# Kernel tuning notes

Measured on AMD Instinct MI355X. Metric: run time of the kernel, lower is better.

Reference implementation:

```python
import jax, jax.numpy as jnp
import numpy as np

B, T, IN, OUT, H, N, M = 16, 1024, 64, 64, 512, 128, 40
EPS = 1e-8


def setup_inputs() -> dict:
    key = jax.random.key(0)
    ks = jax.random.split(key, 16)
    s = 0.02  # xavier-ish init scale for weights
    inp = {
        "x": jax.random.normal(ks[0], (B, T, IN), jnp.float32),
        "h0": jnp.zeros((B, H), jnp.float32),
        "c0": jnp.zeros((B, H), jnp.float32),
        "memory0": jax.random.normal(ks[1], (B, N, M), jnp.float32) * 0.01,
        "read0": jnp.zeros((B, M), jnp.float32),
        # LSTMCell params (torch gate order: i, f, g, o)
        "W_ih": jax.random.normal(ks[2], (4 * H, IN + M), jnp.float32) * s,
        "b_ih": jnp.zeros((4 * H,), jnp.float32),
        "W_hh": jax.random.normal(ks[3], (4 * H, H), jnp.float32) * s,
        "b_hh": jnp.zeros((4 * H,), jnp.float32),
        "W_fc": jax.random.normal(ks[4], (OUT, H), jnp.float32) * s,
        "b_fc": jnp.zeros((OUT,), jnp.float32),
        "W_e": jax.random.normal(ks[5], (M, H), jnp.float32) * s,
        "b_e": jnp.zeros((M,), jnp.float32),
        "W_a": jax.random.normal(ks[6], (M, H), jnp.float32) * s,
        "b_a": jnp.zeros((M,), jnp.float32),
        "W_k": jax.random.normal(ks[7], (M, H), jnp.float32) * s,
        "b_k": jnp.zeros((M,), jnp.float32),
        "W_b": jax.random.normal(ks[8], (1, H), jnp.float32) * s,
        "b_b": jnp.zeros((1,), jnp.float32),
    }
    return inp


def _ntm_scan(x, h0, c0, memory0, read0, W_ih, b_ih, W_hh, b_hh,
              W_fc, b_fc, W_e, b_e, W_a, b_a, W_k, b_k, W_b, b_b):
    def step(carry, x_t):
        h, c, mem, r = carry
        # controller LSTM cell on [x_t, read_vector]
        inp = jnp.concatenate([x_t, r], axis=-1)            # [B, IN+M]
        gates = inp @ W_ih.T + b_ih + h @ W_hh.T + b_hh      # [B, 4H]
        i, f, g, o = jnp.split(gates, 4, axis=-1)
        i = jax.nn.sigmoid(i); f = jax.nn.sigmoid(f)
        g = jnp.tanh(g);       o = jax.nn.sigmoid(o)
        c = f * c + i * g
        h = o * jnp.tanh(c)
        out = jnp.tanh(h @ W_fc.T + b_fc)                    # [B, OUT]
        # content addressing
        key = jnp.tanh(h @ W_k.T + b_k)                      # [B, M]
        beta = jax.nn.softplus(h @ W_b.T + b_b) + EPS        # [B, 1]
        kn = key / (jnp.linalg.norm(key, axis=-1, keepdims=True) + EPS)
        mn = mem / (jnp.linalg.norm(mem, axis=-1, keepdims=True) + EPS)
        sim = jnp.einsum('bnm,bm->bn', mn, kn)               # [B, N]
        w = jax.nn.softmax(beta * sim, axis=-1)              # [B, N]
        # erase/add write, then read from updated memory
        e = jax.nn.sigmoid(h @ W_e.T + b_e)                  # [B, M]
        a = jnp.tanh(h @ W_a.T + b_a)                        # [B, M]
        mem = mem * (1.0 - w[:, :, None] * e[:, None, :]) + w[:, :, None] * a[:, None, :]
        r = jnp.einsum('bn,bnm->bm', w, mem)                 # [B, M]
        return (h, c, mem, r), out

    xs = jnp.swapaxes(x, 0, 1)                               # [T, B, IN]
    (h, c, mem, r), outs = jax.lax.scan(step, (h0, c0, memory0, read0), xs)
    return jnp.swapaxes(outs, 0, 1), h, c                    # [B, T, OUT]


def reference(x, h0, c0, memory0, read0, W_ih, b_ih, W_hh, b_hh,
              W_fc, b_fc, W_e, b_e, W_a, b_a, W_k, b_k, W_b, b_b):
    return _ntm_scan(x, h0, c0, memory0, read0, W_ih, b_ih, W_hh, b_hh,
                     W_fc, b_fc, W_e, b_e, W_a, b_a, W_k, b_k, W_b, b_b)
```

## Files before the change

kernel.cpp:

```cpp
#include <hip/hip_runtime.h>
#include <math.h>

#define Bq   16
#define Tq   1024
#define OUTq 64
#define Hq   512
#define Nq   128
#define Mq   40
#define NT   512
#define NISL 16
#define GWG  13
#define IWG  14
#define NWG  224
#define EPSq 1e-8f
#define MAGIC 0x00C0FFEEu

typedef unsigned long long ull;

__device__ __forceinline__ float sigmf(float x){ return 1.f/(1.f + expf(-x)); }
__device__ __forceinline__ float softplusf(float x){ return (x > 20.f) ? x : log1pf(expf(x)); }

__device__ __forceinline__ ull icld64(const ull* p){
  return __hip_atomic_load(p, __ATOMIC_RELAXED, __HIP_MEMORY_SCOPE_AGENT);
}
__device__ __forceinline__ void icst64(ull* p, ull v){
  __hip_atomic_store(p, v, __ATOMIC_RELAXED, __HIP_MEMORY_SCOPE_AGENT);
}
__device__ __forceinline__ ull icpoll64(const ull* p){
  ull v;
  asm volatile("global_load_dwordx2 %0, %1, off sc0 sc1\n\ts_waitcnt vmcnt(0)"
               : "=v"(v) : "v"(p) : "memory");
  return v;
}
__device__ __forceinline__ ull packtv(unsigned tag, float v){
  return ((ull)tag << 32) | (ull)__float_as_uint(v);
}
__device__ __forceinline__ float lowf(ull v){ return __uint_as_float((unsigned)v); }

__device__ __forceinline__ float waitword(const ull* sh, unsigned want, bool fast){
  if (fast){
    #pragma unroll 1
    for (int i = 0; i < 4096; ++i){
      const ull v = icpoll64(sh);
      if ((unsigned)(v >> 32) == want) return lowf(v);
      __builtin_amdgcn_s_sleep(1);
    }
  }
  #pragma unroll 1
  for (;;){
    const ull v = icld64(sh);
    if ((unsigned)(v >> 32) == want) return lowf(v);
    __builtin_amdgcn_s_sleep(1);
  }
}

__device__ __forceinline__ int ready_and_handshake(ull* rdy, ull* magic, int blk){
  __hip_atomic_fetch_add(rdy, 1ull, __ATOMIC_RELAXED, __HIP_MEMORY_SCOPE_AGENT);
  while (icld64(rdy) < (ull)NWG) __builtin_amdgcn_s_sleep(8);
  if (blk == 0) icst64(magic, ((ull)MAGIC << 32) | 1ull);
  #pragma unroll 1
  for (int i = 0; i < 4000; ++i){
    if ((unsigned)(icpoll64(magic) >> 32) == MAGIC) return 1;
    __builtin_amdgcn_s_sleep(2);
  }
  return 0;
}

extern "C" __global__ void __launch_bounds__(NT, 1)
ntm_kernel(const float* __restrict__ xg,  const float* __restrict__ h0g,
           const float* __restrict__ c0g, const float* __restrict__ mem0g,
           const float* __restrict__ read0g,
           const float* __restrict__ Wih, const float* __restrict__ bih,
           const float* __restrict__ Whh, const float* __restrict__ bhh,
           const float* __restrict__ Wfc, const float* __restrict__ bfc,
           const float* __restrict__ We,  const float* __restrict__ be,
           const float* __restrict__ Wa,  const float* __restrict__ ba,
           const float* __restrict__ Wk,  const float* __restrict__ bk,
           const float* __restrict__ Wb,  const float* __restrict__ bbeta,
           float* __restrict__ yout, ull* __restrict__ rdy,
           ull* __restrict__ h_sh, ull* __restrict__ r_sh,
           ull* __restrict__ hp_sh)
{
  const int blk = blockIdx.x;
  const int tid = threadIdx.x;
  const int x   = blk & 7;
  const int j   = blk >> 3;
  const int bat = (j < IWG) ? x : (x + 8);
  const int slot= (j < IWG) ? j : (j - IWG);
  __shared__ __align__(16) char smem[41344];
  __shared__ int s_fast;
  ull* magic = rdy + 1;

  if (slot < GWG){
    float* inp_s  = (float*)smem;
    float* red_s  = (float*)(smem + 2560);
    float* rw_s   = (float*)(smem + 13440);
    float* r_s    = (float*)(smem + 39680);
    float* gate_s = (float*)(smem + 39840);
    float* c_s    = (float*)(smem + 40480);
    float* bias_s = (float*)(smem + 40640);

    const int kseg  = tid & 15;
    const int rslot = tid >> 4;
    const int nd    = (slot < 12) ? 40 : 32;
    const int d0    = slot * 40;
    const int rowsR = 4 * nd;
    const int prow  = tid >> 2;
    const int pq    = tid & 3;
    const int ncol  = nd >> 2;

    float4 w4[5][9];
    #pragma unroll
    for (int rr = 0; rr < 5; ++rr){
      const int row = rslot*5 + rr;
      if (row < rowsR){
        const int gate = row / nd, ld = row - gate*nd;
        const int grow = gate*Hq + d0 + ld;
        #pragma unroll
        for (int kk = 0; kk < 9; ++kk){
          float v[4];
          #pragma unroll
          for (int c4 = 0; c4 < 4; ++c4){
            const int k = kseg*36 + kk*4 + c4;
            v[c4] = (k < 64) ? Wih[grow*104 + k] : Whh[grow*512 + (k - 64)];
          }
          w4[rr][kk] = make_float4(v[0], v[1], v[2], v[3]);
        }
      } else {
        #pragma unroll
        for (int kk = 0; kk < 9; ++kk) w4[rr][kk] = make_float4(0.f,0.f,0.f,0.f);
      }
    }
    float hw[10];
    #pragma unroll
    for (int c = 0; c < 10; ++c) hw[c] = 0.f;
    if (prow < 121){
      const float* wsrc = (prow < 40) ? (Wk + prow*Hq)
                        : (prow < 80) ? (We + (prow-40)*Hq)
                        : (prow < 120) ? (Wa + (prow-80)*Hq) : Wb;
      #pragma unroll
      for (int c = 0; c < 10; ++c)
        if (c < ncol) hw[c] = wsrc[d0 + pq*ncol + c];
    }
    if (tid < rowsR){
      const int gate = tid / nd, ld = tid - gate*nd;
      const int grow = gate*Hq + d0 + ld;
      bias_s[tid] = bih[grow] + bhh[grow];
    }
    for (int i = tid; i < rowsR*40; i += NT){
      const int row = i / 40, m = i - row*40;
      const int gate = row / nd, ld = row - gate*nd;
      const int grow = gate*Hq + d0 + ld;
      rw_s[row*41 + m] = Wih[grow*104 + 64 + m];
    }
    if (tid < nd) c_s[tid] = c0g[bat*Hq + d0 + tid];
    if (tid < 16)
      *(float4*)&inp_s[tid*4] = ((const float4*)xg)[(bat*Tq + 0)*16 + tid];
    if (tid < 128)
      *(float4*)&inp_s[64 + tid*4] = ((const float4*)h0g)[bat*128 + tid];
    __syncthreads();
    if (tid == 0) s_fast = ready_and_handshake(rdy, magic, blk);
    __syncthreads();
    const bool fast = (s_fast != 0);

    for (int t = 0; t < Tq; ++t){
      const int p = t & 1, pm = (t - 1) & 1;
      float acc[5] = {0.f,0.f,0.f,0.f,0.f};
      {
        const float* bp = inp_s + kseg*36;
        #pragma unroll
        for (int kk = 0; kk < 9; ++kk){
          const float4 f = *(const float4*)&bp[kk*4];
          #pragma unroll
          for (int rr = 0; rr < 5; ++rr)
            acc[rr] += w4[rr][kk].x*f.x + w4[rr][kk].y*f.y
                     + w4[rr][kk].z*f.z + w4[rr][kk].w*f.w;
        }
      }
      #pragma unroll
      for (int rr = 0; rr < 5; ++rr)
        red_s[(rslot*5 + rr)*17 + kseg] = acc[rr];
      if (t == 0){
        if (tid < 40) r_s[tid] = read0g[bat*Mq + tid];
      } else if (tid < 40){
        const int idx = (pm*NISL + bat)*Mq + tid;
        r_s[tid] = waitword(&r_sh[idx], (unsigned)t, fast);
      }
      __syncthreads();
      if (tid < rowsR){
        float s2 = bias_s[tid];
        const float* rp = &red_s[tid*17];
        #pragma unroll
        for (int q = 0; q < 16; ++q) s2 += rp[q];
        const float* rwp = &rw_s[tid*41];
        #pragma unroll
        for (int m = 0; m < 40; ++m) s2 += rwp[m]*r_s[m];
        gate_s[tid] = s2;
      }
      __syncthreads();
      if (tid < nd){
        const float gi = gate_s[tid];
        const float gf = gate_s[nd + tid];
        const float gc = gate_s[2*nd + tid];
        const float go = gate_s[3*nd + tid];
        const float iv = sigmf(gi), fv = sigmf(gf), gv = tanhf(gc), ov = sigmf(go);
        const float cn = fv*c_s[tid] + iv*gv;
        const float hn = ov*tanhf(cn);
        c_s[tid] = cn;
        r_s[tid] = hn;
        const int idx = (p*NISL + bat)*Hq + d0 + tid;
        icst64(&h_sh[idx], packtv((unsigned)(t+1), hn));
        if (t == Tq - 1){
          yout[Bq*Tq*OUTq + bat*Hq + d0 + tid] = hn;
          yout[Bq*Tq*OUTq + Bq*Hq + bat*Hq + d0 + tid] = cn;
        }
      }
      __syncthreads();
      {
        float ps = 0.f;
        #pragma unroll
        for (int c = 0; c < 10; ++c)
          if (c < ncol) ps = fmaf(hw[c], r_s[pq*ncol + c], ps);
        ps += __shfl_xor(ps, 1);
        ps += __shfl_xor(ps, 2);
        if (prow < 121 && pq == 0){
          const int hidx = ((p*NISL + bat)*GWG + slot)*128 + prow;
          icst64(&hp_sh[hidx], packtv((unsigned)(t+1), ps));
        }
      }
      {
        const int idx = (p*NISL + bat)*Hq + tid;
        inp_s[64 + tid] = waitword(&h_sh[idx], (unsigned)(t+1), fast);
      }
      if (t + 1 < Tq && tid < 16)
        *(float4*)&inp_s[tid*4] = ((const float4*)xg)[(bat*Tq + t + 1)*16 + tid];
      __syncthreads();
    }
  }
  else {
    float* mem_s  = (float*)smem;
    float* h_s    = (float*)(smem + 22528);
    float* hred_s = (float*)(smem + 24576);
    float* key_s  = (float*)(smem + 26624);
    float* e_s    = (float*)(smem + 26784);
    float* a_s    = (float*)(smem + 26944);
    float* w_s    = (float*)(smem + 27104);
    float* rred_s = (float*)(smem + 27616);
    float* ored_s = (float*)(smem + 29056);

    #pragma unroll
    for (int q = 0; q < 10; ++q){
      const int e = q*512 + tid;
      const int n = e / 40, m = e - n*40;
      mem_s[n*44 + m] = mem0g[bat*(Nq*Mq) + e];
    }
    const int prow_m = tid & 127;
    const int psg    = tid >> 7;
    float4 wfc[16];
    {
      const int o2 = tid & 63, kc8 = tid >> 6;
      #pragma unroll
      for (int kk = 0; kk < 16; ++kk)
        wfc[kk] = *(const float4*)&Wfc[o2*Hq + kc8*64 + kk*4];
    }
    const float bfcv = bfc[tid & 63];
    float hb0 = 0.f, hb1 = 0.f;
    if (tid < 64){
      const int o0 = tid, o1 = tid + 64;
      hb0 = (o0 < 40) ? bk[o0] : be[o0-40];
      hb1 = (o1 < 80) ? be[o1-40] : (o1 < 120) ? ba[o1-80]
          : (o1 == 120) ? bbeta[0] : 0.f;
    }
    __syncthreads();
    if (tid == 0) s_fast = ready_and_handshake(rdy, magic, blk);
    __syncthreads();
    const bool fast = (s_fast != 0);

    for (int t = 0; t < Tq; ++t){
      const int p = t & 1;
      const unsigned want = (unsigned)(t + 1);
      if (prow_m < 121){
        const int sbase = (psg == 0) ? 0 : (psg*3 + 1);
        const int scnt  = (psg == 0) ? 4 : 3;
        float s = 0.f;
        #pragma unroll
        for (int ss = 0; ss < 4; ++ss){
          if (ss < scnt){
            const int hidx = ((p*NISL + bat)*GWG + (sbase + ss))*128 + prow_m;
            s += waitword(&hp_sh[hidx], want, fast);
          }
        }
        hred_s[prow_m*4 + psg] = s;
      }
      __syncthreads();
      if (tid < 64){
        const int l = tid;
        const float4 p0 = *(const float4*)&hred_s[l*4];
        const float4 p1 = *(const float4*)&hred_s[(l+64)*4];
        float s0 = hb0 + p0.x + p0.y + p0.z + p0.w;
        float s1 = hb1 + p1.x + p1.y + p1.z + p1.w;
        float kv = 0.f;
        if (l < 40){ kv = tanhf(s0); key_s[l] = kv; }
        else        { e_s[l-40] = sigmf(s0); }
        if (l < 16)      e_s[l+24]  = sigmf(s1);
        else if (l < 56) a_s[l-16]  = tanhf(s1);
        float bval = softplusf(s1) + EPSq;
        const float bet = __shfl(bval, 56);
        float ss = kv*kv;
        #pragma unroll
        for (int off = 32; off; off >>= 1) ss += __shfl_xor(ss, off);
        const float rinv = 1.f/(sqrtf(ss) + EPSq);
        float sc[2];
        #pragma unroll
        for (int half = 0; half < 2; ++half){
          const int n = l + 64*half;
          float qq = 0.f, dd = 0.f;
          const float* mrow = &mem_s[n*44];
          #pragma unroll
          for (int q = 0; q < 10; ++q){
            const float4 mv = *(const float4*)&mrow[q*4];
            const float4 kvv = *(const float4*)&key_s[q*4];
            qq += mv.x*mv.x + mv.y*mv.y + mv.z*mv.z + mv.w*mv.w;
            dd += mv.x*kvv.x + mv.y*kvv.y + mv.z*kvv.z + mv.w*kvv.w;
          }
          sc[half] = bet * dd * rinv / (sqrtf(qq) + EPSq);
        }
        const float e0 = expf(sc[0]), e1 = expf(sc[1]);
        float sm = e0 + e1;
        #pragma unroll
        for (int off = 32; off; off >>= 1) sm += __shfl_xor(sm, off);
        const float inv = 1.f/sm;
        w_s[l] = e0*inv; w_s[l+64] = e1*inv;
      }
      __syncthreads();
      if (tid < 320){
        const int m = tid % 40, ng = tid / 40;
        const float ev = e_s[m], av = a_s[m];
        float part = 0.f;
        #pragma unroll
        for (int q = 0; q < 16; ++q){
          const int n = ng*16 + q, idx2 = n*44 + m;
          const float mv = mem_s[idx2];
          const float wn = w_s[n];
          const float nv = fmaf(wn, fmaf(-ev, mv, av), mv);
          mem_s[idx2] = nv;
          part = fmaf(wn, nv, part);
        }
        rred_s[m*9 + ng] = part;
      }
      __syncthreads();
      if (tid < 40){
        float r = 0.f;
        #pragma unroll
        for (int q = 0; q < 8; ++q) r += rred_s[tid*9 + q];
        const int idx = (p*NISL + bat)*Mq + tid;
        icst64(&r_sh[idx], packtv(want, r));
      }
      {
        const int idx = (p*NISL + bat)*Hq + tid;
        h_s[tid] = waitword(&h_sh[idx], want, fast);
      }
      __syncthreads();
      {
        const int o2 = tid & 63, kc8 = tid >> 6;
        float a0 = 0.f;
        const float* hp = h_s + kc8*64;
        #pragma unroll
        for (int kk = 0; kk < 16; ++kk){
          const float4 f = *(const float4*)&hp[kk*4];
          a0 += wfc[kk].x*f.x + wfc[kk].y*f.y + wfc[kk].z*f.z + wfc[kk].w*f.w;
        }
        ored_s[o2*9 + kc8] = a0;
      }
      __syncthreads();
      if (tid < 64){
        float s2 = bfcv;
        const float* op = &ored_s[tid*9];
        #pragma unroll
        for (int q = 0; q < 8; ++q) s2 += op[q];
        yout[(bat*Tq + t)*OUTq + tid] = tanhf(s2);
      }
    }
  }
}

extern "C" void kernel_launch(void* const* d_in, const int* in_sizes, int n_in,
                              void* d_out, int out_size, void* d_ws, size_t ws_size,
                              hipStream_t stream){
  const float* xg    = (const float*)d_in[0];
  const float* h0g   = (const float*)d_in[1];
  const float* c0g   = (const float*)d_in[2];
  const float* mem0g = (const float*)d_in[3];
  const float* read0g= (const float*)d_in[4];
  const float* Wih   = (const float*)d_in[5];
  const float* bih   = (const float*)d_in[6];
  const float* Whh   = (const float*)d_in[7];
  const float* bhh   = (const float*)d_in[8];
  const float* Wfc   = (const float*)d_in[9];
  const float* bfc   = (const float*)d_in[10];
  const float* We    = (const float*)d_in[11];
  const float* be    = (const float*)d_in[12];
  const float* Wa    = (const float*)d_in[13];
  const float* ba    = (const float*)d_in[14];
  const float* Wk    = (const float*)d_in[15];
  const float* bk    = (const float*)d_in[16];
  const float* Wb    = (const float*)d_in[17];
  const float* bbeta = (const float*)d_in[18];

  float* yout  = (float*)d_out;
  ull*   rdy   = (ull*)d_ws;
  ull*   h_sh  = (ull*)((char*)d_ws + 4096);
  ull*   r_sh  = (ull*)((char*)d_ws + 135168);
  ull*   hp_sh = (ull*)((char*)d_ws + 147456);

  hipMemsetAsync(d_ws, 0, 573440, stream);
  hipLaunchKernelGGL(ntm_kernel, dim3(NWG), dim3(NT), 0, stream,
                     xg, h0g, c0g, mem0g, read0g, Wih, bih, Whh, bhh,
                     Wfc, bfc, We, be, Wa, ba, Wk, bk, Wb, bbeta,
                     yout, rdy, h_sh, r_sh, hp_sh);
}
```

Baseline: 6.982 ms.

## Move head weights to LDS and poll head partials concurrently

```diff
diff --git a/kernel.cpp b/kernel.cpp
--- a/kernel.cpp
+++ b/kernel.cpp
@@ -87,7 +87,7 @@
   const int j   = blk >> 3;
   const int bat = (j < IWG) ? x : (x + 8);
   const int slot= (j < IWG) ? j : (j - IWG);
-  __shared__ __align__(16) char smem[41344];
+  __shared__ __align__(16) char smem[62464];
   __shared__ int s_fast;
   ull* magic = rdy + 1;
 
@@ -95,18 +95,18 @@
     float* inp_s  = (float*)smem;
     float* red_s  = (float*)(smem + 2560);
     float* rw_s   = (float*)(smem + 13440);
-    float* r_s    = (float*)(smem + 39680);
-    float* gate_s = (float*)(smem + 39840);
-    float* c_s    = (float*)(smem + 40480);
-    float* bias_s = (float*)(smem + 40640);
+    float* hw_s   = (float*)(smem + 39680);
+    float* r_s    = (float*)(smem + 60672);
+    float* gate_s = (float*)(smem + 60832);
+    float* c_s    = (float*)(smem + 61472);
+    float* bias_s = (float*)(smem + 61632);
+    float* hloc_s = (float*)(smem + 62272);
 
     const int kseg  = tid & 15;
     const int rslot = tid >> 4;
     const int nd    = (slot < 12) ? 40 : 32;
     const int d0    = slot * 40;
     const int rowsR = 4 * nd;
-    const int prow  = tid >> 2;
-    const int pq    = tid & 3;
     const int ncol  = nd >> 2;
 
     float4 w4[5][9];
@@ -131,17 +131,6 @@
         for (int kk = 0; kk < 9; ++kk) w4[rr][kk] = make_float4(0.f,0.f,0.f,0.f);
       }
     }
-    float hw[10];
-    #pragma unroll
-    for (int c = 0; c < 10; ++c) hw[c] = 0.f;
-    if (prow < 121){
-      const float* wsrc = (prow < 40) ? (Wk + prow*Hq)
-                        : (prow < 80) ? (We + (prow-40)*Hq)
-                        : (prow < 120) ? (Wa + (prow-80)*Hq) : Wb;
-      #pragma unroll
-      for (int c = 0; c < 10; ++c)
-        if (c < ncol) hw[c] = wsrc[d0 + pq*ncol + c];
-    }
     if (tid < rowsR){
       const int gate = tid / nd, ld = tid - gate*nd;
       const int grow = gate*Hq + d0 + ld;
@@ -153,7 +142,18 @@
       const int grow = gate*Hq + d0 + ld;
       rw_s[row*41 + m] = Wih[grow*104 + 64 + m];
     }
+    for (int i = tid; i < 128*41; i += NT){
+      const int r = i / 41, m = i - r*41;
+      float v = 0.f;
+      if (r < 121 && m < nd){
+        v = (r < 40) ? Wk[r*Hq + d0 + m]
+          : (r < 80) ? We[(r-40)*Hq + d0 + m]
+          : (r < 120) ? Wa[(r-80)*Hq + d0 + m] : Wb[d0 + m];
+      }
+      hw_s[i] = v;
+    }
     if (tid < nd) c_s[tid] = c0g[bat*Hq + d0 + tid];
+    if (tid < 40) hloc_s[tid] = 0.f;
     if (tid < 16)
       *(float4*)&inp_s[tid*4] = ((const float4*)xg)[(bat*Tq + 0)*16 + tid];
     if (tid < 128)
@@ -207,7 +207,7 @@
         const float cn = fv*c_s[tid] + iv*gv;
         const float hn = ov*tanhf(cn);
         c_s[tid] = cn;
-        r_s[tid] = hn;
+        hloc_s[tid] = hn;
         const int idx = (p*NISL + bat)*Hq + d0 + tid;
         icst64(&h_sh[idx], packtv((unsigned)(t+1), hn));
         if (t == Tq - 1){
@@ -217,15 +217,19 @@
       }
       __syncthreads();
       {
-        float ps = 0.f;
-        #pragma unroll
-        for (int c = 0; c < 10; ++c)
-          if (c < ncol) ps = fmaf(hw[c], r_s[pq*ncol + c], ps);
-        ps += __shfl_xor(ps, 1);
-        ps += __shfl_xor(ps, 2);
-        if (prow < 121 && pq == 0){
-          const int hidx = ((p*NISL + bat)*GWG + slot)*128 + prow;
-          icst64(&hp_sh[hidx], packtv((unsigned)(t+1), ps));
+        const int row = tid >> 2, q = tid & 3;
+        if (row < 121){
+          float ps = 0.f;
+          const float* wp  = &hw_s[row*41 + q*ncol];
+          const float* hp2 = &hloc_s[q*ncol];
+          #pragma unroll
+          for (int c = 0; c < 10; ++c)
+            if (c < ncol) ps = fmaf(wp[c], hp2[c], ps);
+          ps += __shfl_xor(ps, 1);
+          ps += __shfl_xor(ps, 2);
+          if (q == 0)
+            icst64(&hp_sh[((p*NISL + bat)*GWG + slot)*128 + row],
+                   packtv((unsigned)(t+1), ps));
         }
       }
       {
@@ -254,8 +258,6 @@
       const int n = e / 40, m = e - n*40;
       mem_s[n*44 + m] = mem0g[bat*(Nq*Mq) + e];
     }
-    const int prow_m = tid & 127;
-    const int psg    = tid >> 7;
     float4 wfc[16];
     {
       const int o2 = tid & 63, kc8 = tid >> 6;
@@ -279,18 +281,34 @@
     for (int t = 0; t < Tq; ++t){
       const int p = t & 1;
       const unsigned want = (unsigned)(t + 1);
-      if (prow_m < 121){
-        const int sbase = (psg == 0) ? 0 : (psg*3 + 1);
-        const int scnt  = (psg == 0) ? 4 : 3;
+      {
+        const int r = tid & 127, g = tid >> 7;
         float s = 0.f;
-        #pragma unroll
-        for (int ss = 0; ss < 4; ++ss){
-          if (ss < scnt){
-            const int hidx = ((p*NISL + bat)*GWG + (sbase + ss))*128 + prow_m;
-            s += waitword(&hp_sh[hidx], want, fast);
+        if (r < 121){
+          const int scnt = (g == 0) ? 4 : 3;
+          const ull* base = &hp_sh[(p*NISL + bat)*GWG*128];
+          unsigned pend = (1u << scnt) - 1u;
+          float ac[4] = {0.f, 0.f, 0.f, 0.f};
+          int iters = 0;
+          #pragma unroll 1
+          while (pend){
+            #pragma unroll
+            for (int k = 0; k < 4; ++k){
+              if ((pend >> k) & 1){
+                const ull* wp = &base[(g + 4*k)*128 + r];
+                const ull v = (fast && iters < (1 << 16)) ? icpoll64(wp)
+                                                          : icld64(wp);
+                if ((unsigned)(v >> 32) == want){
+                  ac[k] = lowf(v);
+                  pend &= ~(1u << k);
+                }
+              }
+            }
+            if (pend){ __builtin_amdgcn_s_sleep(1); ++iters; }
           }
-        }
-        hred_s[prow_m*4 + psg] = s;
+          s = ac[0] + ac[1] + ac[2] + ac[3];
+        }
+        hred_s[r*4 + g] = s;
       }
       __syncthreads();
       if (tid < 64){
@@ -380,6 +398,7 @@
         for (int q = 0; q < 8; ++q) s2 += op[q];
         yout[(bat*Tq + t)*OUTq + tid] = tanhf(s2);
       }
+      __syncthreads();
     }
   }
 }
```

Result: faster. 6.759 ms (-3.2%).
